# Optimization experiments

Measured on AMD Instinct MI355X. Metric: run time of the kernel, lower is better.

Reference implementation:

```python
import jax, jax.numpy as jnp
import numpy as np
from jax.scipy.linalg import solve_triangular

B, L, HID, H = 2, 2048, 1024, 4
DK, DV = HID // H, HID // H
CHUNK = 32
CONV_K, FIR_SK, FIR_LK, FIR_WK = 4, 3, 31, 64
GIN = HID + 15 * H   # gate mlp input dim
GH = 2 * HID         # fusion_hidden_mult * hidden
FLOOR_INIT = float(np.log(0.05 / 0.95))


def _l2norm(x):
    return x / jnp.sqrt(jnp.sum(x * x, -1, keepdims=True) + 1e-6)


def _dwconv_causal(x_blc, w_ck):
    # x: [B,L,C], w: [C,K] depthwise causal FIR along L
    K = w_ck.shape[-1]
    x = jnp.moveaxis(x_blc, 1, 2)                      # [B,C,L]
    x = jnp.pad(x, ((0, 0), (0, 0), (K - 1, 0)))
    y = jax.lax.conv_general_dilated(x, w_ck[:, None, :], (1,), 'VALID',
                                     feature_group_count=w_ck.shape[0],
                                     dimension_numbers=('NCH', 'OIH', 'NCH'))
    return jnp.moveaxis(y, 2, 1)


def _delta_rule(q, k, v, beta):
    # q,k: [b,h,L,dk]; v: [b,h,L,dv]; beta: [b,h,L]; L % CHUNK == 0
    b, h, Ll, dk = q.shape
    dv = v.shape[-1]
    n = Ll // CHUNK
    q = _l2norm(q); k = _l2norm(k)
    v = v * beta[..., None]
    kb = k * beta[..., None]
    rs = lambda t: t.reshape(b, h, n, CHUNK, t.shape[-1])
    q, k, v, kb = rs(q), rs(k), rs(v), rs(kb)
    tril_strict = jnp.tril(jnp.ones((CHUNK, CHUNK), bool), -1)
    tril = jnp.tril(jnp.ones((CHUNK, CHUNK), bool), 0)
    # strictly-lower part of (k_beta k^T); inv = (I + A)^{-1} (unit lower-triangular)
    A = jnp.where(tril_strict, kb @ jnp.swapaxes(k, -1, -2), 0.0)
    eye = jnp.eye(CHUNK, dtype=q.dtype)
    inv = solve_triangular(eye + A, jnp.broadcast_to(eye, A.shape), lower=True)
    u = inv @ v    # [b,h,n,c,dv]
    w = inv @ kb   # [b,h,n,c,dk]
    qs, ks, us, ws = (jnp.moveaxis(t, 2, 0) for t in (q, k, u, w))
    S0 = jnp.zeros((b, h, dk, dv), q.dtype)

    def step(S, xs):
        q_i, k_i, u_i, w_i = xs
        attn = jnp.where(tril, q_i @ jnp.swapaxes(k_i, -1, -2), 0.0)
        u_adj = u_i - w_i @ S
        o_i = q_i @ S + attn @ u_adj
        S = S + jnp.swapaxes(k_i, -1, -2) @ u_adj
        return S, o_i

    S, o = jax.lax.scan(step, S0, (qs, ks, us, ws))
    o = jnp.moveaxis(o, 0, 2).reshape(b, h, Ll, dv)
    return o, S


def _stats(x):
    # x: [b,l,h,d] -> concat(mean, rms, max_abs) over d -> [b,l,3h]
    mean = x.mean(-1)
    rms = jnp.sqrt(jnp.clip(jnp.mean(x * x, -1), 1e-8))
    mx = jnp.abs(x).max(-1)
    return jnp.concatenate([mean, rms, mx], -1)


def _forward(hidden_states, q_w, k_w, v_w, b_w, convq_w, convk_w, convv_w,
             fir_s, fir_l, fir_wd, g1_w, g1_b, g2_w, g2_b,
             value_bias, log_temp, floor_logit, onorm_w, o_w):
    b, Ll, _ = hidden_states.shape
    # projections + causal short conv + silu (qk_activation='silu')
    q = jax.nn.silu(_dwconv_causal(hidden_states @ q_w.T, convq_w))
    k = jax.nn.silu(_dwconv_causal(hidden_states @ k_w.T, convk_w))
    v = jax.nn.silu(_dwconv_causal(hidden_states @ v_w.T, convv_w))
    tohd = lambda t: t.reshape(b, Ll, H, -1)
    q, k, v = tohd(q), tohd(k), tohd(v)
    beta = jax.nn.sigmoid(hidden_states @ b_w.T)            # [b,l,h]
    tr = lambda t: jnp.moveaxis(t, 1, 2)
    delta_out, _S = _delta_rule(tr(q), tr(k), tr(v), jnp.moveaxis(beta, 1, 2))
    delta_out = jnp.moveaxis(delta_out, 1, 2)               # [b,l,h,dv]
    # per-head depthwise FIR branches on v
    def fir(x, filt):
        y = _dwconv_causal(x.reshape(b, Ll, H * DV), filt.reshape(H * DV, -1))
        return y.reshape(b, Ll, H, DV)
    short, long_, wide = fir(v, fir_s), fir(v, fir_l), fir(v, fir_wd)
    gate_in = jnp.concatenate([hidden_states, _stats(short), _stats(long_),
                               _stats(wide), _stats(delta_out), _stats(v)], -1)
    hdn = jax.nn.gelu(gate_in @ g1_w.T + g1_b, approximate=False)
    logits = (hdn @ g2_w.T + g2_b).reshape(b, Ll, H, 5)
    logits = logits.at[..., 4].add(value_bias)              # value-branch bias
    logits = logits / jnp.exp(log_temp)[None, None, :, None]
    p = jax.nn.softmax(logits, -1)
    # adaptive floor: context branches each guaranteed >= f per head
    f = jax.nn.sigmoid(floor_logit)[None, None, :, None]    # [1,1,h,1]
    scale = 1.0 - 4.0 * f
    w_ctx = f + scale * p[..., :4]
    w_val = scale * p[..., 4:5]
    o = (w_ctx[..., 0:1] * short + w_ctx[..., 1:2] * long_ +
         w_ctx[..., 2:3] * wide + w_ctx[..., 3:4] * delta_out + w_val * v)
    # per-head RMSNorm + output proj
    o = o * jax.lax.rsqrt(jnp.mean(o * o, -1, keepdims=True) + 1e-5) * onorm_w
    return o.reshape(b, Ll, HID) @ o_w.T


def setup_inputs() -> dict:
    key = jax.random.key(0)
    ks = jax.random.split(key, 16)
    rn = lambda i, shp, s: jax.random.normal(ks[i], shp, jnp.float32) * s
    fir_init = lambda i, K: jnp.zeros((H, DV, K), jnp.float32).at[..., -1].set(1.0) + rn(i, (H, DV, K), 0.02)
    g2_b = jnp.zeros((5 * H,), jnp.float32).at[4::5].set(4.0)
    return {
        'hidden_states': jax.random.normal(ks[0], (B, L, HID), jnp.float32),
        'q_w': rn(1, (HID, HID), 0.02), 'k_w': rn(2, (HID, HID), 0.02),
        'v_w': rn(3, (HID, HID), 0.02), 'b_w': rn(4, (H, HID), 0.02),
        'convq_w': rn(5, (HID, CONV_K), 0.2), 'convk_w': rn(6, (HID, CONV_K), 0.2),
        'convv_w': rn(7, (HID, CONV_K), 0.2),
        'fir_s': fir_init(8, FIR_SK), 'fir_l': fir_init(9, FIR_LK), 'fir_wd': fir_init(10, FIR_WK),
        'g1_w': rn(11, (GH, GIN), 0.02), 'g1_b': jnp.zeros((GH,), jnp.float32),
        'g2_w': rn(12, (5 * H, GH), 0.02), 'g2_b': g2_b,
        'value_bias': jnp.full((H,), 4.0, jnp.float32),
        'log_temp': jnp.zeros((H,), jnp.float32),
        'floor_logit': jnp.full((H,), FLOOR_INIT, jnp.float32),
        'onorm_w': jnp.ones((DV,), jnp.float32),
        'o_w': rn(13, (HID, HID), 0.02),
    }


def reference(hidden_states, q_w, k_w, v_w, b_w, convq_w, convk_w, convv_w,
              fir_s, fir_l, fir_wd, g1_w, g1_b, g2_w, g2_b,
              value_bias, log_temp, floor_logit, onorm_w, o_w):
    return _forward(hidden_states, q_w, k_w, v_w, b_w, convq_w, convk_w, convv_w,
                    fir_s, fir_l, fir_wd, g1_w, g1_b, g2_w, g2_b,
                    value_bias, log_temp, floor_logit, onorm_w, o_w)
```

## Files before the change

kernel.cpp:

```cpp
#include <hip/hip_runtime.h>

#define B_ 2
#define L_ 2048
#define HID_ 1024
#define H_ 4
#define D_ 256
#define NTOK 4096
#define CH 32
#define NCH 64

typedef short s16x8 __attribute__((ext_vector_type(8)));
typedef float f32x4 __attribute__((ext_vector_type(4)));
typedef unsigned short u16;
typedef unsigned int u32;

__device__ __forceinline__ u16 f2b(float f) {
  u32 u = __float_as_uint(f);
  u32 r = (u + 0x7fffu + ((u >> 16) & 1u)) >> 16;
  return (u16)r;
}
__device__ __forceinline__ float b2f(u16 h) { return __uint_as_float((u32)h << 16); }
__device__ __forceinline__ float blo(u32 u) { return __uint_as_float(u << 16); }
__device__ __forceinline__ float bhi(u32 u) { return __uint_as_float(u & 0xffff0000u); }

union U4S8 { uint4 u; s16x8 s; };
__device__ __forceinline__ s16x8 as_s16x8(uint4 u) { U4S8 x; x.u = u; return x.s; }

__global__ __launch_bounds__(256)
void cast_bf(const float* __restrict__ in, u16* __restrict__ out, int n)
{
  int id = (blockIdx.x * 256 + threadIdx.x) * 4;
  if (id >= n) return;
  float4 v = *(const float4*)(in + id);
  ushort4 o;
  o.x = f2b(v.x); o.y = f2b(v.y); o.z = f2b(v.z); o.w = f2b(v.w);
  *(ushort4*)(out + id) = o;
}

template<int ACT>
__global__ __launch_bounds__(256)
void gemm_bf16(const u16* __restrict__ A, const u16* __restrict__ W,
               const float* __restrict__ bias, float* __restrict__ C,
               int M, int N, int K)
{
  __shared__ u16 Als[128][64];
  __shared__ u16 Bls[128][64];
  const int tid = threadIdx.x;
  const int n0 = blockIdx.x * 128;
  const int m0 = blockIdx.y * 128;
  const int l = tid & 63, w = tid >> 6;
  const int wm = w >> 1, wn = w & 1;
  const int r15 = l & 15, g = l >> 4;
  const int srow = tid >> 1, sh = tid & 1;

  f32x4 acc[4][4];
#pragma unroll
  for (int i = 0; i < 4; i++)
#pragma unroll
    for (int j = 0; j < 4; j++) acc[i][j] = (f32x4){0.f, 0.f, 0.f, 0.f};

  const long arowoff = (long)(m0 + srow) * K + sh * 32;
  const long browoff = (long)(n0 + srow) * K + sh * 32;
  uint4 ra[4], rb[4];
#pragma unroll
  for (int j2 = 0; j2 < 4; j2++) {
    ra[j2] = *(const uint4*)(A + arowoff + j2 * 8);
    rb[j2] = *(const uint4*)(W + browoff + j2 * 8);
  }
  const int NS = K >> 6;
  for (int s = 0; s < NS; ++s) {
    __syncthreads();
#pragma unroll
    for (int j2 = 0; j2 < 4; j2++) {
      int slot = (sh * 4 + j2) ^ (srow & 7);
      *(uint4*)&Als[srow][slot * 8] = ra[j2];
      *(uint4*)&Bls[srow][slot * 8] = rb[j2];
    }
    __syncthreads();
    if (s + 1 < NS) {
      long k0 = (long)(s + 1) * 64;
#pragma unroll
      for (int j2 = 0; j2 < 4; j2++) {
        ra[j2] = *(const uint4*)(A + arowoff + k0 + j2 * 8);
        rb[j2] = *(const uint4*)(W + browoff + k0 + j2 * 8);
      }
    }
#pragma unroll
    for (int kk2 = 0; kk2 < 2; kk2++) {
      s16x8 af[4], bf[4];
      int slot = ((kk2 * 4 + g) ^ (r15 & 7)) * 8;
#pragma unroll
      for (int mt = 0; mt < 4; mt++)
        af[mt] = *(const s16x8*)&Als[64 * wm + mt * 16 + r15][slot];
#pragma unroll
      for (int nt = 0; nt < 4; nt++)
        bf[nt] = *(const s16x8*)&Bls[64 * wn + nt * 16 + r15][slot];
#pragma unroll
      for (int mt = 0; mt < 4; mt++)
#pragma unroll
        for (int nt = 0; nt < 4; nt++)
          acc[mt][nt] = __builtin_amdgcn_mfma_f32_16x16x32_bf16(af[mt], bf[nt], acc[mt][nt], 0, 0, 0);
    }
  }

#pragma unroll
  for (int mt = 0; mt < 4; mt++) {
#pragma unroll
    for (int nt = 0; nt < 4; nt++) {
      int m = m0 + 64 * wm + mt * 16 + g * 4;
      int n = n0 + 64 * wn + nt * 16 + r15;
      float bv = (ACT == 1) ? bias[n] : 0.f;
#pragma unroll
      for (int r = 0; r < 4; r++) {
        float v = acc[mt][nt][r];
        if (ACT == 1) {
          v += bv;
          v = 0.5f * v * (1.f + erff(v * 0.70710678118654752f));
        }
        C[(long)(m + r) * N + n] = v;
      }
    }
  }
}

__global__ __launch_bounds__(256)
void conv4_silu(const float* __restrict__ x, const float* __restrict__ w4,
                float* __restrict__ y)
{
  int id = blockIdx.x * 256 + threadIdx.x;
  int c = id & (HID_ - 1);
  int tok = id >> 10;
  int l = tok & (L_ - 1);
  float s = 0.f;
#pragma unroll
  for (int t = 0; t < 4; t++) {
    int lt = l - 3 + t;
    if (lt >= 0) s += x[(long)(tok - 3 + t) * HID_ + c] * w4[c * 4 + t];
  }
  y[id] = s / (1.f + expf(-s));
}

__global__ __launch_bounds__(256)
void beta_proj(const float* __restrict__ hs, const float* __restrict__ bw,
               float* __restrict__ beta)
{
  int id = blockIdx.x * 256 + threadIdx.x;
  int h = id & 3;
  int tok = id >> 2;
  const float4* a = (const float4*)(hs + (long)tok * HID_);
  const float4* w = (const float4*)(bw + (long)h * HID_);
  float s = 0.f;
  for (int k = 0; k < HID_ / 4; k++) {
    float4 av = a[k], wv = w[k];
    s += av.x * wv.x + av.y * wv.y + av.z * wv.z + av.w * wv.w;
  }
  beta[id] = 1.f / (1.f + expf(-s));
}

__global__ __launch_bounds__(256)
void pad_g1w(const float* __restrict__ g1w, u16* __restrict__ out)
{
  int id = blockIdx.x * 256 + threadIdx.x;
  int k = id % 1088;
  int n = id / 1088;
  out[id] = (k < 1084) ? f2b(g1w[(long)n * 1084 + k]) : (u16)0;
}

__global__ __launch_bounds__(256)
void delta_prep(const float* __restrict__ qc, const float* __restrict__ kc,
                const float* __restrict__ vc, const float* __restrict__ beta,
                u16* __restrict__ qn, u16* __restrict__ ktb,
                float* __restrict__ ub, u16* __restrict__ wb,
                u16* __restrict__ attnb, u16* __restrict__ attnlo)
{
  __shared__ float qs[CH][260], ks[CH][260], vs[CH][260];
  __shared__ float Xs[CH][33], As[CH][33];
  __shared__ float red[CH][8];
  __shared__ float bet[CH], nf[CH];

  int bid = blockIdx.x;
  int ci = bid & 63, h = (bid >> 6) & 3, b = bid >> 8;
  int tid = threadIdx.x;
  long tok0 = (long)b * L_ + (long)ci * CH;
  const float* qsrc = qc + tok0 * HID_ + h * D_;
  const float* ksrc = kc + tok0 * HID_ + h * D_;
  const float* vsrc = vc + tok0 * HID_ + h * D_;
  int lr = tid >> 6;
  int dd = (tid & 63) << 2;

#pragma unroll
  for (int it = 0; it < 8; it++) {
    int row = lr + it * 4;
    *(float4*)&qs[row][dd] = *(const float4*)(qsrc + (long)row * HID_ + dd);
    *(float4*)&ks[row][dd] = *(const float4*)(ksrc + (long)row * HID_ + dd);
    *(float4*)&vs[row][dd] = *(const float4*)(vsrc + (long)row * HID_ + dd);
  }
  if (tid < CH) bet[tid] = beta[(tok0 + tid) * H_ + h];
  __syncthreads();

  {
    int c = tid >> 3, p = tid & 7;
    float s = 0.f;
    for (int d = p * 32; d < p * 32 + 32; d++) { float v = qs[c][d]; s += v * v; }
    red[c][p] = s;
  }
  __syncthreads();
  if (tid < CH) {
    float s = 0.f;
    for (int p = 0; p < 8; p++) s += red[tid][p];
    nf[tid] = rsqrtf(s + 1e-6f);
  }
  __syncthreads();
#pragma unroll
  for (int it = 0; it < 8; it++) {
    int row = lr + it * 4;
    float f = nf[row];
    qs[row][dd] *= f; qs[row][dd + 1] *= f; qs[row][dd + 2] *= f; qs[row][dd + 3] *= f;
  }
  {
    int c = tid >> 3, p = tid & 7;
    float s = 0.f;
    for (int d = p * 32; d < p * 32 + 32; d++) { float v = ks[c][d]; s += v * v; }
    red[c][p] = s;
  }
  __syncthreads();
  if (tid < CH) {
    float s = 0.f;
    for (int p = 0; p < 8; p++) s += red[tid][p];
    nf[tid] = rsqrtf(s + 1e-6f);
  }
  __syncthreads();
#pragma unroll
  for (int it = 0; it < 8; it++) {
    int row = lr + it * 4;
    float f = nf[row];
    ks[row][dd] *= f; ks[row][dd + 1] *= f; ks[row][dd + 2] *= f; ks[row][dd + 3] *= f;
  }
  __syncthreads();

  long abase = ((long)(b * H_ + h) * NCH + ci) * (CH * CH);
#pragma unroll 1
  for (int r = 0; r < 4; r++) {
    int oid = tid + 256 * r;
    int i = oid >> 5, jj = oid & 31;
    float skk = 0.f, sqk = 0.f;
    for (int d = 0; d < D_; d += 4) {
      float4 ki = *(const float4*)&ks[i][d];
      float4 kj = *(const float4*)&ks[jj][d];
      float4 qi = *(const float4*)&qs[i][d];
      skk += ki.x * kj.x + ki.y * kj.y + ki.z * kj.z + ki.w * kj.w;
      sqk += qi.x * kj.x + qi.y * kj.y + qi.z * kj.z + qi.w * kj.w;
    }
    As[i][jj] = (jj < i) ? bet[i] * skk : 0.f;
    float sv = (jj <= i) ? sqk : 0.f;
    u16 hi16 = f2b(sv);
    attnb[abase + oid] = hi16;
    attnlo[abase + oid] = f2b(sv - b2f(hi16));
  }
  __syncthreads();

  if (tid < CH) {
    int jj = tid;
    for (int i = 0; i < CH; i++) {
      if (i < jj) { Xs[i][jj] = 0.f; continue; }
      float x = (i == jj) ? 1.f : 0.f;
      for (int m = jj; m < i; m++) x -= As[i][m] * Xs[m][jj];
      Xs[i][jj] = x;
    }
  }
  __syncthreads();

#pragma unroll
  for (int r = 0; r < 4; r++) {
    int oid = tid + 256 * r;
    int i = oid >> 5, m = oid & 31;
    As[i][m] = Xs[i][m] * bet[m];
  }
  __syncthreads();

  long cbase = ((long)(b * H_ + h) * NCH + ci) * (CH * D_);
#pragma unroll 1
  for (int c = 0; c < CH; c++) {
    float su = 0.f, sw = 0.f;
    for (int m = 0; m < CH; m++) {
      float xm = As[c][m];
      su = fmaf(xm, vs[m][tid], su);
      sw = fmaf(xm, ks[m][tid], sw);
    }
    ub[cbase + c * D_ + tid] = su;
    wb[cbase + c * D_ + tid] = f2b(sw);
  }
#pragma unroll 1
  for (int i = 0; i < CH; i++) {
    qn[cbase + i * D_ + tid] = f2b(qs[i][tid]);
  }
  {
    u32 pk[16];
#pragma unroll
    for (int c2 = 0; c2 < 16; c2++) {
      float a = ks[2 * c2][tid], b2 = ks[2 * c2 + 1][tid];
      asm("v_cvt_pk_bf16_f32 %0, %1, %2" : "=v"(pk[c2]) : "v"(a), "v"(b2));
    }
    u16* kq = ktb + ((long)(b * H_ + h) * NCH + ci) * (D_ * CH) + (long)tid * CH;
    *(uint4*)(kq + 0)  = make_uint4(pk[0], pk[1], pk[2], pk[3]);
    *(uint4*)(kq + 8)  = make_uint4(pk[4], pk[5], pk[6], pk[7]);
    *(uint4*)(kq + 16) = make_uint4(pk[8], pk[9], pk[10], pk[11]);
    *(uint4*)(kq + 24) = make_uint4(pk[12], pk[13], pk[14], pk[15]);
  }
}

__device__ __forceinline__ void d2b2(f32x4 Ta, f32x4 Tb, int v, int hi,
                                     s16x8* hiF, s16x8* loF)
{
  const bool tb = (hi >> 1) != 0;
  const int base = v + ((hi & 1) << 5);
  float y[8];
#pragma unroll
  for (int r = 0; r < 4; r++) {
    float a0 = __shfl(Ta[r], base);
    float b0 = __shfl(Tb[r], base);
    float a1 = __shfl(Ta[r], base + 16);
    float b1 = __shfl(Tb[r], base + 16);
    y[r] = tb ? b0 : a0;
    y[4 + r] = tb ? b1 : a1;
  }
  u32 h0, h1, h2, h3;
  asm("v_cvt_pk_bf16_f32 %0, %1, %2" : "=v"(h0) : "v"(y[0]), "v"(y[1]));
  asm("v_cvt_pk_bf16_f32 %0, %1, %2" : "=v"(h1) : "v"(y[2]), "v"(y[3]));
  asm("v_cvt_pk_bf16_f32 %0, %1, %2" : "=v"(h2) : "v"(y[4]), "v"(y[5]));
  asm("v_cvt_pk_bf16_f32 %0, %1, %2" : "=v"(h3) : "v"(y[6]), "v"(y[7]));
  float z0 = y[0] - blo(h0), z1 = y[1] - bhi(h0);
  float z2 = y[2] - blo(h1), z3 = y[3] - bhi(h1);
  float z4 = y[4] - blo(h2), z5 = y[5] - bhi(h2);
  float z6 = y[6] - blo(h3), z7 = y[7] - bhi(h3);
  u32 l0, l1, l2, l3;
  asm("v_cvt_pk_bf16_f32 %0, %1, %2" : "=v"(l0) : "v"(z0), "v"(z1));
  asm("v_cvt_pk_bf16_f32 %0, %1, %2" : "=v"(l1) : "v"(z2), "v"(z3));
  asm("v_cvt_pk_bf16_f32 %0, %1, %2" : "=v"(l2) : "v"(z4), "v"(z5));
  asm("v_cvt_pk_bf16_f32 %0, %1, %2" : "=v"(l3) : "v"(z6), "v"(z7));
  U4S8 xh; xh.u = make_uint4(h0, h1, h2, h3);
  U4S8 xl; xl.u = make_uint4(l0, l1, l2, l3);
  *hiF = xh.s; *loF = xl.s;
}

__global__ __launch_bounds__(64, 1)
void delta_scan(const u16* __restrict__ qn, const u16* __restrict__ ktb,
                const float* __restrict__ ub, const u16* __restrict__ wb,
                const u16* __restrict__ attnb, const u16* __restrict__ attnlo,
                float* __restrict__ dout)
{
  const int bid = blockIdx.x;
  const int sl = bid & 15, h = (bid >> 4) & 3, b = bid >> 6;
  const int l = threadIdx.x;
  const int v = l & 15, hi = l >> 4;
  const int dv0 = sl * 16;
  const long bh = (long)(b * H_ + h);

  f32x4 St[16];
#pragma unroll
  for (int t = 0; t < 16; t++) St[t] = (f32x4){0.f, 0.f, 0.f, 0.f};

#pragma unroll 1
  for (int ci = 0; ci < NCH; ci++) {
    const long cb = (bh * NCH + ci) * (CH * D_);
    const long kb = (bh * NCH + ci) * (D_ * CH);
    const long ab = (bh * NCH + ci) * (CH * CH);

    uint4 Wf[2][8], Qf[2][8], KTf[16], ATh[2], ATl[2];
    float Uld[2][4];
#pragma unroll
    for (int mt = 0; mt < 2; mt++)
#pragma unroll
      for (int kt = 0; kt < 8; kt++) {
        const long ro = cb + (long)(mt * 16 + v) * D_ + kt * 32 + hi * 8;
        Wf[mt][kt] = *(const uint4*)(wb + ro);
        Qf[mt][kt] = *(const uint4*)(qn + ro);
      }
#pragma unroll
    for (int t = 0; t < 16; t++)
      KTf[t] = *(const uint4*)(ktb + kb + (long)(t * 16 + v) * CH + hi * 8);
#pragma unroll
    for (int mt = 0; mt < 2; mt++) {
      ATh[mt] = *(const uint4*)(attnb + ab + (long)(mt * 16 + v) * CH + hi * 8);
      ATl[mt] = *(const uint4*)(attnlo + ab + (long)(mt * 16 + v) * CH + hi * 8);
    }
#pragma unroll
    for (int mt = 0; mt < 2; mt++)
#pragma unroll
      for (int r = 0; r < 4; r++)
        Uld[mt][r] = ub[cb + (long)(mt * 16 + hi * 4 + r) * D_ + dv0 + v];

    s16x8 Sbh[8], Sbl[8];
#pragma unroll
    for (int kt = 0; kt < 8; kt++)
      d2b2(St[2 * kt], St[2 * kt + 1], v, hi, &Sbh[kt], &Sbl[kt]);

    f32x4 awt[2], aqt[2];
#pragma unroll
    for (int mt = 0; mt < 2; mt++) { awt[mt] = (f32x4){0.f,0.f,0.f,0.f}; aqt[mt] = (f32x4){0.f,0.f,0.f,0.f}; }
#pragma unroll
    for (int kt = 0; kt < 8; kt++) {
#pragma unroll
      for (int mt = 0; mt < 2; mt++) {
        awt[mt] = __builtin_amdgcn_mfma_f32_16x16x32_bf16(as_s16x8(Wf[mt][kt]), Sbh[kt], awt[mt], 0, 0, 0);
        awt[mt] = __builtin_amdgcn_mfma_f32_16x16x32_bf16(as_s16x8(Wf[mt][kt]), Sbl[kt], awt[mt], 0, 0, 0);
        aqt[mt] = __builtin_amdgcn_mfma_f32_16x16x32_bf16(as_s16x8(Qf[mt][kt]), Sbh[kt], aqt[mt], 0, 0, 0);
        aqt[mt] = __builtin_amdgcn_mfma_f32_16x16x32_bf16(as_s16x8(Qf[mt][kt]), Sbl[kt], aqt[mt], 0, 0, 0);
      }
    }

    f32x4 ua0, ua1;
#pragma unroll
    for (int r = 0; r < 4; r++) { ua0[r] = Uld[0][r] - awt[0][r]; ua1[r] = Uld[1][r] - awt[1][r]; }
    s16x8 UAh, UAl;
    d2b2(ua0, ua1, v, hi, &UAh, &UAl);

    f32x4 ot[2];
#pragma unroll
    for (int mt = 0; mt < 2; mt++) {
      ot[mt] = __builtin_amdgcn_mfma_f32_16x16x32_bf16(as_s16x8(ATh[mt]), UAh, aqt[mt], 0, 0, 0);
      ot[mt] = __builtin_amdgcn_mfma_f32_16x16x32_bf16(as_s16x8(ATh[mt]), UAl, ot[mt], 0, 0, 0);
      ot[mt] = __builtin_amdgcn_mfma_f32_16x16x32_bf16(as_s16x8(ATl[mt]), UAh, ot[mt], 0, 0, 0);
    }
#pragma unroll
    for (int mt = 0; mt < 2; mt++)
#pragma unroll
      for (int r = 0; r < 4; r++)
        dout[((long)b * L_ + ci * CH + mt * 16 + hi * 4 + r) * HID_ + h * D_ + dv0 + v] = ot[mt][r];

#pragma unroll
    for (int t = 0; t < 16; t++) {
      St[t] = __builtin_amdgcn_mfma_f32_16x16x32_bf16(as_s16x8(KTf[t]), UAh, St[t], 0, 0, 0);
      St[t] = __builtin_amdgcn_mfma_f32_16x16x32_bf16(as_s16x8(KTf[t]), UAl, St[t], 0, 0, 0);
    }
  }
}

__global__ __launch_bounds__(256)
void fir3(const float* __restrict__ v, const float* __restrict__ fs_g,
          const float* __restrict__ fl_g, const float* __restrict__ fw_g,
          float* __restrict__ os, float* __restrict__ ol, float* __restrict__ ow)
{
  __shared__ float xs[95][64];
  __shared__ float fs[64][3];
  __shared__ float fl[64][31];
  __shared__ float fw[64][65];
  int bid = blockIdx.x;
  int ct = bid & 15, lt = bid >> 4;
  int c0 = ct * 64, tok0 = lt * 32;
  int bstart = (tok0 / L_) * L_;
  int tid = threadIdx.x;

  for (int idx = tid; idx < 95 * 64; idx += 256) {
    int r = idx >> 6, cc = idx & 63;
    int tok = tok0 - 63 + r;
    xs[r][cc] = (tok >= bstart) ? v[(long)tok * HID_ + c0 + cc] : 0.f;
  }
  for (int idx = tid; idx < 64 * 3; idx += 256) fs[idx / 3][idx % 3] = fs_g[(long)(c0 + idx / 3) * 3 + idx % 3];
  for (int idx = tid; idx < 64 * 31; idx += 256) fl[idx / 31][idx % 31] = fl_g[(long)(c0 + idx / 31) * 31 + idx % 31];
  for (int idx = tid; idx < 64 * 64; idx += 256) fw[idx >> 6][idx & 63] = fw_g[(long)(c0 + (idx >> 6)) * 64 + (idx & 63)];
  __syncthreads();

  int cc = tid & 63, lq = tid >> 6;
  int rb = lq * 8;
  float as8[8] = {0}, al8[8] = {0}, aw8[8] = {0};
#pragma unroll 1
  for (int t = 0; t < 64; t++) {
    float fv = fw[cc][t];
#pragma unroll
    for (int i = 0; i < 8; i++) aw8[i] = fmaf(xs[rb + i + t][cc], fv, aw8[i]);
  }
#pragma unroll 1
  for (int t = 0; t < 31; t++) {
    float fv = fl[cc][t];
#pragma unroll
    for (int i = 0; i < 8; i++) al8[i] = fmaf(xs[rb + 33 + i + t][cc], fv, al8[i]);
  }
#pragma unroll 1
  for (int t = 0; t < 3; t++) {
    float fv = fs[cc][t];
#pragma unroll
    for (int i = 0; i < 8; i++) as8[i] = fmaf(xs[rb + 61 + i + t][cc], fv, as8[i]);
  }
#pragma unroll
  for (int i = 0; i < 8; i++) {
    long o = (long)(tok0 + lq * 8 + i) * HID_ + c0 + cc;
    os[o] = as8[i]; ol[o] = al8[i]; ow[o] = aw8[i];
  }
}

__global__ __launch_bounds__(256)
void build_gate(const float* __restrict__ hs, const float* __restrict__ sb,
                const float* __restrict__ lb, const float* __restrict__ wbb,
                const float* __restrict__ db, const float* __restrict__ vb,
                u16* __restrict__ gate)
{
  int tok = blockIdx.x;
  int tid = threadIdx.x;
  u16* g = gate + (long)tok * 1088;
  const float* hrow = hs + (long)tok * HID_;
#pragma unroll
  for (int i = 0; i < 4; i++) g[tid + 256 * i] = f2b(hrow[tid + 256 * i]);
  if (tid < 4) g[1084 + tid] = 0;
  int h = tid >> 6, ln = tid & 63;
  const float* brs[5] = {sb, lb, wbb, db, vb};
#pragma unroll
  for (int bi = 0; bi < 5; bi++) {
    const float* x = brs[bi] + (long)tok * HID_ + h * D_;
    float s = 0.f, ss = 0.f, mx = 0.f;
#pragma unroll
    for (int i = 0; i < 4; i++) {
      float v = x[ln + 64 * i];
      s += v; ss += v * v; mx = fmaxf(mx, fabsf(v));
    }
#pragma unroll
    for (int off = 32; off >= 1; off >>= 1) {
      s += __shfl_xor(s, off);
      ss += __shfl_xor(ss, off);
      mx = fmaxf(mx, __shfl_xor(mx, off));
    }
    if (ln == 0) {
      g[1024 + bi * 12 + h] = f2b(s * (1.f / 256.f));
      g[1024 + bi * 12 + 4 + h] = f2b(sqrtf(fmaxf(ss * (1.f / 256.f), 1e-8f)));
      g[1024 + bi * 12 + 8 + h] = f2b(mx);
    }
  }
}

__global__ __launch_bounds__(256)
void g2_mix(const float* __restrict__ hdn, const float* __restrict__ g2w,
            const float* __restrict__ g2b, const float* __restrict__ vbias,
            const float* __restrict__ ltemp, const float* __restrict__ flog,
            const float* __restrict__ onw,
            const float* __restrict__ sb, const float* __restrict__ lb,
            const float* __restrict__ wbb, const float* __restrict__ db,
            const float* __restrict__ vb, u16* __restrict__ omix)
{
  __shared__ float hrow[2048];
  __shared__ float lg[20];
  int tok = blockIdx.x;
  int tid = threadIdx.x;
  const float* hp = hdn + (long)tok * 2048;
#pragma unroll
  for (int i = 0; i < 8; i++) hrow[tid + 256 * i] = hp[tid + 256 * i];
  __syncthreads();
  int w = tid >> 6, ln = tid & 63;
#pragma unroll 1
  for (int q = 0; q < 5; q++) {
    int jj = w * 5 + q;
    const float* wr = g2w + (long)jj * 2048;
    float s = 0.f;
    for (int i = 0; i < 32; i++) s += hrow[ln + 64 * i] * wr[ln + 64 * i];
#pragma unroll
    for (int off = 32; off >= 1; off >>= 1) s += __shfl_xor(s, off);
    if (ln == 0) lg[jj] = s + g2b[jj];
  }
  __syncthreads();
  int h = w;
  float l[5];
#pragma unroll
  for (int j = 0; j < 5; j++) l[j] = lg[h * 5 + j];
  l[4] += vbias[h];
  float it = expf(-ltemp[h]);
#pragma unroll
  for (int j = 0; j < 5; j++) l[j] *= it;
  float mx = fmaxf(fmaxf(fmaxf(l[0], l[1]), fmaxf(l[2], l[3])), l[4]);
  float e[5], se = 0.f;
#pragma unroll
  for (int j = 0; j < 5; j++) { e[j] = expf(l[j] - mx); se += e[j]; }
  float inv = 1.f / se;
  float f = 1.f / (1.f + expf(-flog[h]));
  float sc = 1.f - 4.f * f;
  float wt[5];
#pragma unroll
  for (int j = 0; j < 4; j++) wt[j] = f + sc * e[j] * inv;
  wt[4] = sc * e[4] * inv;

  long base = (long)tok * HID_ + h * D_;
  float o[4], ss = 0.f;
#pragma unroll
  for (int i = 0; i < 4; i++) {
    int d = ln + 64 * i;
    o[i] = wt[0] * sb[base + d] + wt[1] * lb[base + d] + wt[2] * wbb[base + d]
         + wt[3] * db[base + d] + wt[4] * vb[base + d];
    ss += o[i] * o[i];
  }
#pragma unroll
  for (int off = 32; off >= 1; off >>= 1) ss += __shfl_xor(ss, off);
  float r = rsqrtf(ss * (1.f / 256.f) + 1e-5f);
#pragma unroll
  for (int i = 0; i < 4; i++) {
    int d = ln + 64 * i;
    omix[base + d] = f2b(o[i] * r * onw[d]);
  }
}

extern "C" void kernel_launch(void* const* d_in, const int* in_sizes, int n_in,
                              void* d_out, int out_size, void* d_ws, size_t ws_size,
                              hipStream_t stream)
{
  const float* hs    = (const float*)d_in[0];
  const float* q_w   = (const float*)d_in[1];
  const float* k_w   = (const float*)d_in[2];
  const float* v_w   = (const float*)d_in[3];
  const float* b_w   = (const float*)d_in[4];
  const float* convq = (const float*)d_in[5];
  const float* convk = (const float*)d_in[6];
  const float* convv = (const float*)d_in[7];
  const float* fir_s = (const float*)d_in[8];
  const float* fir_l = (const float*)d_in[9];
  const float* fir_w = (const float*)d_in[10];
  const float* g1w   = (const float*)d_in[11];
  const float* g1b   = (const float*)d_in[12];
  const float* g2w   = (const float*)d_in[13];
  const float* g2b   = (const float*)d_in[14];
  const float* vbias = (const float*)d_in[15];
  const float* ltemp = (const float*)d_in[16];
  const float* flog  = (const float*)d_in[17];
  const float* onw   = (const float*)d_in[18];
  const float* o_w   = (const float*)d_in[19];

  float* ws = (float*)d_ws;
  const long S1 = (long)NTOK * HID_;
  float* qp     = ws + 0 * S1;
  float* kp     = ws + 1 * S1;
  float* vp     = ws + 2 * S1;
  float* qcv    = ws + 3 * S1;
  float* kcv    = ws + 4 * S1;
  float* vcv    = ws + 5 * S1;
  float* ubb    = ws + 6 * S1;
  float* deltab = ws + 7 * S1;
  u16*   qn_bf  = (u16*)(ws + 8 * S1);
  u16*   kt_bf  = (u16*)(ws + 8 * S1 + S1 / 2);
  u16*   wb_bf  = (u16*)(ws + 9 * S1);
  u16*   attn_bf = (u16*)(ws + 9 * S1 + S1 / 2);
  float* betab  = (float*)(attn_bf + (long)B_ * H_ * NCH * CH * CH);
  u16*   attn_lo = (u16*)(betab + 16384);
  u16*   hs_bf  = (u16*)(ws + 10 * S1);
  u16*   qw_bf  = (u16*)(ws + 10 * S1 + S1 / 2);
  u16*   kw_bf  = qw_bf + S1 / 4;
  u16*   vw_bf  = kw_bf + S1 / 4;
  u16*   ow_bf  = vw_bf + S1 / 4;
  u16*   g1w_bf = ow_bf + S1 / 4;
  u16*   gate_bf = (u16*)qcv;
  u16*   omix_bf = (u16*)kcv;
  float* hdnb    = ws + 8 * S1;
  (void)in_sizes; (void)n_in; (void)out_size; (void)ws_size;

  dim3 blk(256);
  cast_bf<<<(NTOK * HID_) / 1024, blk, 0, stream>>>(hs, hs_bf, NTOK * HID_);
  cast_bf<<<(HID_ * HID_) / 1024, blk, 0, stream>>>(q_w, qw_bf, HID_ * HID_);
  cast_bf<<<(HID_ * HID_) / 1024, blk, 0, stream>>>(k_w, kw_bf, HID_ * HID_);
  cast_bf<<<(HID_ * HID_) / 1024, blk, 0, stream>>>(v_w, vw_bf, HID_ * HID_);
  cast_bf<<<(HID_ * HID_) / 1024, blk, 0, stream>>>(o_w, ow_bf, HID_ * HID_);
  pad_g1w<<<2048 * 1088 / 256, blk, 0, stream>>>(g1w, g1w_bf);
  gemm_bf16<0><<<dim3(8, 32), blk, 0, stream>>>(hs_bf, qw_bf, nullptr, qp, NTOK, HID_, HID_);
  gemm_bf16<0><<<dim3(8, 32), blk, 0, stream>>>(hs_bf, kw_bf, nullptr, kp, NTOK, HID_, HID_);
  gemm_bf16<0><<<dim3(8, 32), blk, 0, stream>>>(hs_bf, vw_bf, nullptr, vp, NTOK, HID_, HID_);
  conv4_silu<<<NTOK * HID_ / 256, blk, 0, stream>>>(qp, convq, qcv);
  conv4_silu<<<NTOK * HID_ / 256, blk, 0, stream>>>(kp, convk, kcv);
  conv4_silu<<<NTOK * HID_ / 256, blk, 0, stream>>>(vp, convv, vcv);
  beta_proj<<<NTOK * H_ / 256, blk, 0, stream>>>(hs, b_w, betab);
  delta_prep<<<B_ * H_ * NCH, blk, 0, stream>>>(qcv, kcv, vcv, betab, qn_bf, kt_bf, ubb, wb_bf, attn_bf, attn_lo);
  delta_scan<<<B_ * H_ * 16, dim3(64), 0, stream>>>(qn_bf, kt_bf, ubb, wb_bf, attn_bf, attn_lo, deltab);
  fir3<<<(NTOK / 32) * (HID_ / 64), blk, 0, stream>>>(vcv, fir_s, fir_l, fir_w, qp, kp, vp);
  build_gate<<<NTOK, blk, 0, stream>>>(hs, qp, kp, vp, deltab, vcv, gate_bf);
  gemm_bf16<1><<<dim3(16, 32), blk, 0, stream>>>(gate_bf, g1w_bf, g1b, hdnb, NTOK, 2048, 1088);
  g2_mix<<<NTOK, blk, 0, stream>>>(hdnb, g2w, g2b, vbias, ltemp, flog, onw,
                                   qp, kp, vp, deltab, vcv, omix_bf);
  gemm_bf16<0><<<dim3(8, 32), blk, 0, stream>>>(omix_bf, ow_bf, nullptr, (float*)d_out, NTOK, HID_, HID_);
}
```

Baseline: 954.7 us.

## Fuse QKV GEMM, casts and convs; prefetch next chunk in delta scan

Measured after the change: 886.7 us. 1.08x faster.

```diff
diff --git a/kernel.cpp b/kernel.cpp
--- a/kernel.cpp
+++ b/kernel.cpp
@@ -27,11 +27,20 @@
 __device__ __forceinline__ s16x8 as_s16x8(uint4 u) { U4S8 x; x.u = u; return x.s; }
 
 __global__ __launch_bounds__(256)
-void cast_bf(const float* __restrict__ in, u16* __restrict__ out, int n)
-{
-  int id = (blockIdx.x * 256 + threadIdx.x) * 4;
-  if (id >= n) return;
-  float4 v = *(const float4*)(in + id);
+void cast5(const float* __restrict__ hs, const float* __restrict__ qw,
+           const float* __restrict__ kw, const float* __restrict__ vw,
+           const float* __restrict__ ow, u16* __restrict__ out)
+{
+  const long M4 = (long)NTOK * HID_;
+  const long M1 = (long)HID_ * HID_;
+  long id = ((long)blockIdx.x * 256 + threadIdx.x) * 4;
+  const float* src; long off;
+  if (id < M4)               { src = hs; off = id; }
+  else if (id < M4 + M1)     { src = qw; off = id - M4; }
+  else if (id < M4 + 2 * M1) { src = kw; off = id - M4 - M1; }
+  else if (id < M4 + 3 * M1) { src = vw; off = id - M4 - 2 * M1; }
+  else                       { src = ow; off = id - M4 - 3 * M1; }
+  float4 v = *(const float4*)(src + off);
   ushort4 o;
   o.x = f2b(v.x); o.y = f2b(v.y); o.z = f2b(v.z); o.w = f2b(v.w);
   *(ushort4*)(out + id) = o;
@@ -124,20 +133,25 @@
 }
 
 __global__ __launch_bounds__(256)
-void conv4_silu(const float* __restrict__ x, const float* __restrict__ w4,
-                float* __restrict__ y)
-{
-  int id = blockIdx.x * 256 + threadIdx.x;
-  int c = id & (HID_ - 1);
-  int tok = id >> 10;
+void conv4_silu3(const float* __restrict__ qkv, const float* __restrict__ wq,
+                 const float* __restrict__ wk, const float* __restrict__ wv,
+                 float* __restrict__ yq, float* __restrict__ yk, float* __restrict__ yv)
+{
+  long id = (long)blockIdx.x * 256 + threadIdx.x;
+  int col = (int)(id % 3072);
+  int tok = (int)(id / 3072);
+  int g = col >> 10, c = col & 1023;
   int l = tok & (L_ - 1);
+  const float* w4 = (g == 0 ? wq : g == 1 ? wk : wv) + c * 4;
   float s = 0.f;
 #pragma unroll
   for (int t = 0; t < 4; t++) {
     int lt = l - 3 + t;
-    if (lt >= 0) s += x[(long)(tok - 3 + t) * HID_ + c] * w4[c * 4 + t];
-  }
-  y[id] = s / (1.f + expf(-s));
+    if (lt >= 0) s += qkv[(long)(tok - 3 + t) * 3072 + col] * w4[t];
+  }
+  float r = s / (1.f + expf(-s));
+  float* y = (g == 0 ? yq : g == 1 ? yk : yv);
+  y[(long)tok * HID_ + c] = r;
 }
 
 __global__ __launch_bounds__(256)
@@ -360,25 +374,30 @@
 #pragma unroll
   for (int t = 0; t < 16; t++) St[t] = (f32x4){0.f, 0.f, 0.f, 0.f};
 
-#pragma unroll 1
-  for (int ci = 0; ci < NCH; ci++) {
+  uint4 WfA[2][8], QfA[2][8], WfB[2][8], QfB[2][8];
+  uint4 KTf[16], ATh[2], ATl[2];
+  float Uld[2][4];
+
+  auto loadWQ = [&](uint4 (&W)[2][8], uint4 (&Q)[2][8], int ci) {
     const long cb = (bh * NCH + ci) * (CH * D_);
-    const long kb = (bh * NCH + ci) * (D_ * CH);
-    const long ab = (bh * NCH + ci) * (CH * CH);
-
-    uint4 Wf[2][8], Qf[2][8], KTf[16], ATh[2], ATl[2];
-    float Uld[2][4];
 #pragma unroll
     for (int mt = 0; mt < 2; mt++)
 #pragma unroll
       for (int kt = 0; kt < 8; kt++) {
         const long ro = cb + (long)(mt * 16 + v) * D_ + kt * 32 + hi * 8;
-        Wf[mt][kt] = *(const uint4*)(wb + ro);
-        Qf[mt][kt] = *(const uint4*)(qn + ro);
+        W[mt][kt] = *(const uint4*)(wb + ro);
+        Q[mt][kt] = *(const uint4*)(qn + ro);
       }
+  };
+  auto loadKT = [&](int ci) {
+    const long kb = (bh * NCH + ci) * (D_ * CH);
 #pragma unroll
     for (int t = 0; t < 16; t++)
       KTf[t] = *(const uint4*)(ktb + kb + (long)(t * 16 + v) * CH + hi * 8);
+  };
+  auto loadATU = [&](int ci) {
+    const long ab = (bh * NCH + ci) * (CH * CH);
+    const long cb = (bh * NCH + ci) * (CH * D_);
 #pragma unroll
     for (int mt = 0; mt < 2; mt++) {
       ATh[mt] = *(const uint4*)(attnb + ab + (long)(mt * 16 + v) * CH + hi * 8);
@@ -389,23 +408,25 @@
 #pragma unroll
       for (int r = 0; r < 4; r++)
         Uld[mt][r] = ub[cb + (long)(mt * 16 + hi * 4 + r) * D_ + dv0 + v];
-
-    s16x8 Sbh[8], Sbl[8];
-#pragma unroll
-    for (int kt = 0; kt < 8; kt++)
-      d2b2(St[2 * kt], St[2 * kt + 1], v, hi, &Sbh[kt], &Sbl[kt]);
+  };
+
+  auto step = [&](uint4 (&CW)[2][8], uint4 (&CQ)[2][8],
+                  uint4 (&NW)[2][8], uint4 (&NQ)[2][8], int ci) {
+    loadWQ(NW, NQ, ci + 1);
 
     f32x4 awt[2], aqt[2];
 #pragma unroll
     for (int mt = 0; mt < 2; mt++) { awt[mt] = (f32x4){0.f,0.f,0.f,0.f}; aqt[mt] = (f32x4){0.f,0.f,0.f,0.f}; }
 #pragma unroll
     for (int kt = 0; kt < 8; kt++) {
+      s16x8 sh_, sl_;
+      d2b2(St[2 * kt], St[2 * kt + 1], v, hi, &sh_, &sl_);
 #pragma unroll
       for (int mt = 0; mt < 2; mt++) {
-        awt[mt] = __builtin_amdgcn_mfma_f32_16x16x32_bf16(as_s16x8(Wf[mt][kt]), Sbh[kt], awt[mt], 0, 0, 0);
-        awt[mt] = __builtin_amdgcn_mfma_f32_16x16x32_bf16(as_s16x8(Wf[mt][kt]), Sbl[kt], awt[mt], 0, 0, 0);
-        aqt[mt] = __builtin_amdgcn_mfma_f32_16x16x32_bf16(as_s16x8(Qf[mt][kt]), Sbh[kt], aqt[mt], 0, 0, 0);
-        aqt[mt] = __builtin_amdgcn_mfma_f32_16x16x32_bf16(as_s16x8(Qf[mt][kt]), Sbl[kt], aqt[mt], 0, 0, 0);
+        awt[mt] = __builtin_amdgcn_mfma_f32_16x16x32_bf16(as_s16x8(CW[mt][kt]), sh_, awt[mt], 0, 0, 0);
+        awt[mt] = __builtin_amdgcn_mfma_f32_16x16x32_bf16(as_s16x8(CW[mt][kt]), sl_, awt[mt], 0, 0, 0);
+        aqt[mt] = __builtin_amdgcn_mfma_f32_16x16x32_bf16(as_s16x8(CQ[mt][kt]), sh_, aqt[mt], 0, 0, 0);
+        aqt[mt] = __builtin_amdgcn_mfma_f32_16x16x32_bf16(as_s16x8(CQ[mt][kt]), sl_, aqt[mt], 0, 0, 0);
       }
     }
 
@@ -428,11 +449,23 @@
       for (int r = 0; r < 4; r++)
         dout[((long)b * L_ + ci * CH + mt * 16 + hi * 4 + r) * HID_ + h * D_ + dv0 + v] = ot[mt][r];
 
+    loadATU(ci + 1);
+
 #pragma unroll
     for (int t = 0; t < 16; t++) {
       St[t] = __builtin_amdgcn_mfma_f32_16x16x32_bf16(as_s16x8(KTf[t]), UAh, St[t], 0, 0, 0);
       St[t] = __builtin_amdgcn_mfma_f32_16x16x32_bf16(as_s16x8(KTf[t]), UAl, St[t], 0, 0, 0);
     }
+    loadKT(ci + 1);
+  };
+
+  loadWQ(WfA, QfA, 0);
+  loadKT(0);
+  loadATU(0);
+#pragma unroll 1
+  for (int c2 = 0; c2 < NCH / 2; c2++) {
+    step(WfA, QfA, WfB, QfB, 2 * c2);
+    step(WfB, QfB, WfA, QfA, 2 * c2 + 1);
   }
 }
 
@@ -622,9 +655,7 @@
 
   float* ws = (float*)d_ws;
   const long S1 = (long)NTOK * HID_;
-  float* qp     = ws + 0 * S1;
-  float* kp     = ws + 1 * S1;
-  float* vp     = ws + 2 * S1;
+  float* qkv3   = ws + 0 * S1;
   float* qcv    = ws + 3 * S1;
   float* kcv    = ws + 4 * S1;
   float* vcv    = ws + 5 * S1;
@@ -638,35 +669,28 @@
   u16*   attn_lo = (u16*)(betab + 16384);
   u16*   hs_bf  = (u16*)(ws + 10 * S1);
   u16*   qw_bf  = (u16*)(ws + 10 * S1 + S1 / 2);
-  u16*   kw_bf  = qw_bf + S1 / 4;
-  u16*   vw_bf  = kw_bf + S1 / 4;
-  u16*   ow_bf  = vw_bf + S1 / 4;
+  u16*   ow_bf  = qw_bf + 3 * (S1 / 4);
   u16*   g1w_bf = ow_bf + S1 / 4;
+  float* firs = ws + 0 * S1;
+  float* firl = ws + 1 * S1;
+  float* firw = ws + 2 * S1;
   u16*   gate_bf = (u16*)qcv;
   u16*   omix_bf = (u16*)kcv;
   float* hdnb    = ws + 8 * S1;
   (void)in_sizes; (void)n_in; (void)out_size; (void)ws_size;
 
   dim3 blk(256);
-  cast_bf<<<(NTOK * HID_) / 1024, blk, 0, stream>>>(hs, hs_bf, NTOK * HID_);
-  cast_bf<<<(HID_ * HID_) / 1024, blk, 0, stream>>>(q_w, qw_bf, HID_ * HID_);
-  cast_bf<<<(HID_ * HID_) / 1024, blk, 0, stream>>>(k_w, kw_bf, HID_ * HID_);
-  cast_bf<<<(HID_ * HID_) / 1024, blk, 0, stream>>>(v_w, vw_bf, HID_ * HID_);
-  cast_bf<<<(HID_ * HID_) / 1024, blk, 0, stream>>>(o_w, ow_bf, HID_ * HID_);
+  cast5<<<(NTOK * HID_ + 4 * HID_ * HID_) / 1024, blk, 0, stream>>>(hs, q_w, k_w, v_w, o_w, hs_bf);
   pad_g1w<<<2048 * 1088 / 256, blk, 0, stream>>>(g1w, g1w_bf);
-  gemm_bf16<0><<<dim3(8, 32), blk, 0, stream>>>(hs_bf, qw_bf, nullptr, qp, NTOK, HID_, HID_);
-  gemm_bf16<0><<<dim3(8, 32), blk, 0, stream>>>(hs_bf, kw_bf, nullptr, kp, NTOK, HID_, HID_);
-  gemm_bf16<0><<<dim3(8, 32), blk, 0, stream>>>(hs_bf, vw_bf, nullptr, vp, NTOK, HID_, HID_);
-  conv4_silu<<<NTOK * HID_ / 256, blk, 0, stream>>>(qp, convq, qcv);
-  conv4_silu<<<NTOK * HID_ / 256, blk, 0, stream>>>(kp, convk, kcv);
-  conv4_silu<<<NTOK * HID_ / 256, blk, 0, stream>>>(vp, convv, vcv);
+  gemm_bf16<0><<<dim3(24, 32), blk, 0, stream>>>(hs_bf, qw_bf, nullptr, qkv3, NTOK, 3072, HID_);
+  conv4_silu3<<<(NTOK * 3072) / 256, blk, 0, stream>>>(qkv3, convq, convk, convv, qcv, kcv, vcv);
   beta_proj<<<NTOK * H_ / 256, blk, 0, stream>>>(hs, b_w, betab);
   delta_prep<<<B_ * H_ * NCH, blk, 0, stream>>>(qcv, kcv, vcv, betab, qn_bf, kt_bf, ubb, wb_bf, attn_bf, attn_lo);
   delta_scan<<<B_ * H_ * 16, dim3(64), 0, stream>>>(qn_bf, kt_bf, ubb, wb_bf, attn_bf, attn_lo, deltab);
-  fir3<<<(NTOK / 32) * (HID_ / 64), blk, 0, stream>>>(vcv, fir_s, fir_l, fir_w, qp, kp, vp);
-  build_gate<<<NTOK, blk, 0, stream>>>(hs, qp, kp, vp, deltab, vcv, gate_bf);
+  fir3<<<(NTOK / 32) * (HID_ / 64), blk, 0, stream>>>(vcv, fir_s, fir_l, fir_w, firs, firl, firw);
+  build_gate<<<NTOK, blk, 0, stream>>>(hs, firs, firl, firw, deltab, vcv, gate_bf);
   gemm_bf16<1><<<dim3(16, 32), blk, 0, stream>>>(gate_bf, g1w_bf, g1b, hdnb, NTOK, 2048, 1088);
   g2_mix<<<NTOK, blk, 0, stream>>>(hdnb, g2w, g2b, vbias, ltemp, flog, onw,
-                                   qp, kp, vp, deltab, vcv, omix_bf);
+                                   firs, firl, firw, deltab, vcv, omix_bf);
   gemm_bf16<0><<<dim3(8, 32), blk, 0, stream>>>(omix_bf, ow_bf, nullptr, (float*)d_out, NTOK, HID_, HID_);
 }
```
